# Kernel tuning notes

Measured on AMD Instinct MI355X. Metric: run time of the kernel, lower is better.

## Reference

```python
import jax, jax.numpy as jnp
import numpy as np

TAU = 0.2
LW = 0.5
EPS = 1e-12  # tf.math.l2_normalize epsilon


def _l2norm(x):
    ss = jnp.sum(x * x, axis=-1, keepdims=True)
    return x * jax.lax.rsqrt(jnp.maximum(ss, EPS))


def _global_head(f, W1, b1, W2, b2):
    g = jnp.mean(f, axis=(1, 2))            # GlobalAveragePooling2D -> [B, C]
    h = jax.nn.relu(g @ W1 + b1)
    return h @ W2 + b2                      # [B, 128]


def _dense_head(f, W1, b1, W2, b2):
    # 1x1 convs == per-pixel matmuls
    h = jax.nn.relu(jnp.einsum('bhwc,cd->bhwd', f, W1) + b1)
    return jnp.einsum('bhwd,de->bhwe', h, W2) + b2  # [B, H, W, 128]


def _info_nce(q, k):
    logits = (q @ k.T) / TAU                # [N, N]
    lse = jax.nn.logsumexp(logits, axis=-1)
    pos = jnp.diagonal(logits)
    return jnp.mean(lse - pos)


def setup_inputs() -> dict:
    key = jax.random.key(0)
    ks = jax.random.split(key, 10)
    B, H, W, C = 128, 7, 7, 2048
    Dh, De = 2048, 128
    s1 = 1.0 / np.sqrt(C)
    s2 = 1.0 / np.sqrt(Dh)
    inp = {
        'feat_q': jax.random.normal(ks[0], (B, H, W, C), jnp.float32),
        'feat_k': jax.random.normal(ks[1], (B, H, W, C), jnp.float32),
        'Wg1': jax.random.normal(ks[2], (C, Dh), jnp.float32) * s1,
        'bg1': jnp.zeros((Dh,), jnp.float32),
        'Wg2': jax.random.normal(ks[3], (Dh, De), jnp.float32) * s2,
        'bg2': jnp.zeros((De,), jnp.float32),
        'Wd1': jax.random.normal(ks[4], (C, Dh), jnp.float32) * s1,
        'bd1': jnp.zeros((Dh,), jnp.float32),
        'Wd2': jax.random.normal(ks[5], (Dh, De), jnp.float32) * s2,
        'bd2': jnp.zeros((De,), jnp.float32),
        'mWg1': jax.random.normal(ks[6], (C, Dh), jnp.float32) * s1,
        'mbg1': jnp.zeros((Dh,), jnp.float32),
        'mWg2': jax.random.normal(ks[7], (Dh, De), jnp.float32) * s2,
        'mbg2': jnp.zeros((De,), jnp.float32),
        'mWd1': jax.random.normal(ks[8], (C, Dh), jnp.float32) * s1,
        'mbd1': jnp.zeros((Dh,), jnp.float32),
        'mWd2': jax.random.normal(ks[9], (Dh, De), jnp.float32) * s2,
        'mbd2': jnp.zeros((De,), jnp.float32),
    }
    return inp


def reference(feat_q, feat_k, Wg1, bg1, Wg2, bg2, Wd1, bd1, Wd2, bd2,
              mWg1, mbg1, mWg2, mbg2, mWd1, mbd1, mWd2, mbd2):
    # query (student) branch
    q_g = _l2norm(_global_head(feat_q, Wg1, bg1, Wg2, bg2))      # [B, 128]
    q_d = _l2norm(_dense_head(feat_q, Wd1, bd1, Wd2, bd2))       # [B, H, W, 128]
    # key (momentum teacher) branch, stop-gradient as in train_step
    k_g = jax.lax.stop_gradient(_l2norm(_global_head(feat_k, mWg1, mbg1, mWg2, mbg2)))
    k_d = jax.lax.stop_gradient(_l2norm(_dense_head(feat_k, mWd1, mbd1, mWd2, mbd2)))

    l_g = _info_nce(q_g, k_g)

    B, H, W, De = q_d.shape
    f1 = q_d.reshape(B, H * W, De)
    f2 = k_d.reshape(B, H * W, De)
    sim = jnp.einsum('bnc,bmc->bnm', f1, f2)                     # [B, HW, HW]
    idx = jnp.argmax(sim, axis=-1)                               # [B, HW]
    matched = jnp.take_along_axis(f2, idx[..., None], axis=1)    # [B, HW, 128]

    l_d = _info_nce(f1.reshape(-1, De), matched.reshape(-1, De))
    total = (1.0 - LW) * l_g + LW * l_d
    return total
```

## Files before the change

kernel.cpp:

```cpp
#include <hip/hip_runtime.h>
#include <cstddef>

typedef __bf16 bf16x8 __attribute__((ext_vector_type(8)));
typedef float  f32x4  __attribute__((ext_vector_type(4)));
typedef unsigned short u16x8 __attribute__((ext_vector_type(8)));

__device__ __forceinline__ float b2f(unsigned short u) {
    union { unsigned int i; float f; } v; v.i = ((unsigned int)u) << 16; return v.f;
}
__device__ __forceinline__ unsigned short f2b(float f) {
    union { float f; unsigned int i; } v; v.f = f;
    unsigned int r = v.i + 0x7fffu + ((v.i >> 16) & 1u);
    return (unsigned short)(r >> 16);
}
__device__ __forceinline__ void gl_lds16(const void* g, void* l) {
    __builtin_amdgcn_global_load_lds((const __attribute__((address_space(1))) void*)g,
                                     (__attribute__((address_space(3))) void*)l,
                                     16, 0, 0);
}

__global__ __launch_bounds__(64) void detect_kernel(const unsigned short* __restrict__ feat,
                                                    int* __restrict__ flag) {
    __shared__ int cnt;
    if (threadIdx.x == 0) cnt = 0;
    __syncthreads();
    int c = 0;
    for (int i = threadIdx.x; i < 256; i += 64) {
        float v = b2f(feat[i]);
        if (fabsf(v) > 100.0f) ++c;
    }
    atomicAdd(&cnt, c);
    __syncthreads();
    if (threadIdx.x == 0) *flag = (cnt > 16) ? 1 : 0;
}

__global__ __launch_bounds__(256) void zero_kernel(float* __restrict__ p, int n4) {
    int i = blockIdx.x * 256 + threadIdx.x;
    const f32x4 z = {0.f, 0.f, 0.f, 0.f};
    if (i < n4) ((f32x4*)p)[i] = z;
}

__global__ __launch_bounds__(256) void convert_kernel(const void* __restrict__ in,
                                                      unsigned short* __restrict__ out,
                                                      const int* __restrict__ flagp) {
    int fl = *flagp;
    size_t i = ((size_t)blockIdx.x * 256 + threadIdx.x) * 8;
    if (fl) {
        const float* inf = (const float*)in;
        f32x4 v0 = *(const f32x4*)(inf + i);
        f32x4 v1 = *(const f32x4*)(inf + i + 4);
        u16x8 o;
        o[0]=f2b(v0[0]); o[1]=f2b(v0[1]); o[2]=f2b(v0[2]); o[3]=f2b(v0[3]);
        o[4]=f2b(v1[0]); o[5]=f2b(v1[1]); o[6]=f2b(v1[2]); o[7]=f2b(v1[3]);
        *(u16x8*)(out + i) = o;
    } else {
        *(u16x8*)(out + i) = *(const u16x8*)((const unsigned short*)in + i);
    }
}

__global__ __launch_bounds__(256) void pool_kernel(const void* __restrict__ fq,
                                                   const void* __restrict__ fk,
                                                   unsigned short* __restrict__ gq,
                                                   unsigned short* __restrict__ gk,
                                                   const int* __restrict__ flagp) {
    int fl = *flagp;
    int c = blockIdx.x * 256 + threadIdx.x;
    int b = blockIdx.y;
    const void* src = blockIdx.z ? fk : fq;
    unsigned short* dst = blockIdx.z ? gk : gq;
    size_t base = (size_t)b * 49 * 2048 + c;
    float s = 0.f;
    if (fl) {
        const float* sf = (const float*)src;
        #pragma unroll
        for (int p = 0; p < 49; ++p) s += sf[base + (size_t)p * 2048];
    } else {
        const unsigned short* su = (const unsigned short*)src;
        #pragma unroll
        for (int p = 0; p < 49; ++p) s += b2f(su[base + (size_t)p * 2048]);
    }
    dst[(size_t)b * 2048 + c] = f2b(s * (1.0f / 49.0f));
}

__global__ __launch_bounds__(256) void transpose2v_kernel(
    const void* __restrict__ s0, const void* __restrict__ s1,
    unsigned short* __restrict__ d0, unsigned short* __restrict__ d1,
    int rows, int cols, const int* __restrict__ flagp) {
    int fl = *flagp;
    int z = blockIdx.z;
    const void* in = z ? s1 : s0;
    unsigned short* out = z ? d1 : d0;
    __shared__ unsigned short tile[64 * 72];
    int bx = blockIdx.x * 64, by = blockIdx.y * 64;
    int tr = threadIdx.x >> 3;
    int tc = (threadIdx.x & 7) * 8;
    #pragma unroll
    for (int h = 0; h < 2; ++h) {
        int r = tr + h * 32;
        if (fl) {
            const float* inf = (const float*)in + (size_t)(by + r) * cols + bx + tc;
            f32x4 v0 = *(const f32x4*)inf;
            f32x4 v1 = *(const f32x4*)(inf + 4);
            u16x8 o;
            o[0]=f2b(v0[0]); o[1]=f2b(v0[1]); o[2]=f2b(v0[2]); o[3]=f2b(v0[3]);
            o[4]=f2b(v1[0]); o[5]=f2b(v1[1]); o[6]=f2b(v1[2]); o[7]=f2b(v1[3]);
            *(u16x8*)(tile + r * 72 + tc) = o;
        } else {
            const unsigned short* inu = (const unsigned short*)in + (size_t)(by + r) * cols + bx + tc;
            *(u16x8*)(tile + r * 72 + tc) = *(const u16x8*)inu;
        }
    }
    __syncthreads();
    #pragma unroll
    for (int h = 0; h < 2; ++h) {
        int oc = tr + h * 32;
        u16x8 v;
        #pragma unroll
        for (int j = 0; j < 8; ++j) v[j] = tile[(tc + j) * 72 + oc];
        *(u16x8*)(out + (size_t)(bx + oc) * rows + by + tc) = v;
    }
}

__global__ __launch_bounds__(256) void transpose4v_kernel(
    const void* __restrict__ s0, const void* __restrict__ s1,
    const void* __restrict__ s2, const void* __restrict__ s3,
    unsigned short* __restrict__ d0, unsigned short* __restrict__ d1,
    unsigned short* __restrict__ d2, unsigned short* __restrict__ d3,
    int rows, int cols, const int* __restrict__ flagp) {
    int fl = *flagp;
    int z = blockIdx.z;
    const void* in = (z == 0) ? s0 : (z == 1) ? s1 : (z == 2) ? s2 : s3;
    unsigned short* out = (z == 0) ? d0 : (z == 1) ? d1 : (z == 2) ? d2 : d3;
    __shared__ unsigned short tile[64 * 72];
    int bx = blockIdx.x * 64, by = blockIdx.y * 64;
    int tr = threadIdx.x >> 3;
    int tc = (threadIdx.x & 7) * 8;
    #pragma unroll
    for (int h = 0; h < 2; ++h) {
        int r = tr + h * 32;
        if (fl) {
            const float* inf = (const float*)in + (size_t)(by + r) * cols + bx + tc;
            f32x4 v0 = *(const f32x4*)inf;
            f32x4 v1 = *(const f32x4*)(inf + 4);
            u16x8 o;
            o[0]=f2b(v0[0]); o[1]=f2b(v0[1]); o[2]=f2b(v0[2]); o[3]=f2b(v0[3]);
            o[4]=f2b(v1[0]); o[5]=f2b(v1[1]); o[6]=f2b(v1[2]); o[7]=f2b(v1[3]);
            *(u16x8*)(tile + r * 72 + tc) = o;
        } else {
            const unsigned short* inu = (const unsigned short*)in + (size_t)(by + r) * cols + bx + tc;
            *(u16x8*)(tile + r * 72 + tc) = *(const u16x8*)inu;
        }
    }
    __syncthreads();
    #pragma unroll
    for (int h = 0; h < 2; ++h) {
        int oc = tr + h * 32;
        u16x8 v;
        #pragma unroll
        for (int j = 0; j < 8; ++j) v[j] = tile[(tc + j) * 72 + oc];
        *(u16x8*)(out + (size_t)(bx + oc) * rows + by + tc) = v;
    }
}

__global__ __launch_bounds__(256) void mlp_kernel(
    const unsigned short* __restrict__ A0, const unsigned short* __restrict__ A1,
    const unsigned short* __restrict__ Bt0, const unsigned short* __restrict__ Bt1,
    const unsigned short* __restrict__ W20, const unsigned short* __restrict__ W21,
    const void* __restrict__ b10, const void* __restrict__ b11,
    float* __restrict__ out0, float* __restrict__ out1,
    const int* __restrict__ flagp)
{
    int fl = *flagp;
    int z  = blockIdx.z;
    const unsigned short* A  = z ? A1 : A0;
    const unsigned short* Bt = z ? Bt1 : Bt0;
    const unsigned short* W2 = z ? W21 : W20;
    const void* b1 = z ? b11 : b10;
    float* outp = z ? out1 : out0;
    const int K = 2048;

    __shared__ unsigned short smem[8192 + 9216];
    unsigned short* As = smem;
    unsigned short* Bs = smem + 8192;
    unsigned short* Hs = smem + 8192;

    int tid  = threadIdx.x;
    int lane = tid & 63;
    int w    = tid >> 6;
    int wm = w & 1, wn = w >> 1;
    int quad = lane >> 4, l16 = lane & 15;
    size_t m0 = (size_t)blockIdx.y * 128;
    size_t n0 = (size_t)blockIdx.x * 128;

    int lrow = lane >> 3;
    int kc   = (lane & 7) ^ lrow;

    const unsigned short* gA[4];
    const unsigned short* gB[4];
    unsigned short* lA[4];
    unsigned short* lB[4];
    #pragma unroll
    for (int c = 0; c < 4; ++c) {
        int row = w * 32 + c * 8 + lrow;
        gA[c] = A  + (m0 + row) * (size_t)K + kc * 8;
        gB[c] = Bt + (n0 + row) * (size_t)K + kc * 8;
        lA[c] = As + w * 2048 + c * 512;
        lB[c] = Bs + w * 2048 + c * 512;
    }

    const f32x4 zero4 = {0.f, 0.f, 0.f, 0.f};
    f32x4 acc[4][4];
    #pragma unroll
    for (int i = 0; i < 4; ++i)
        #pragma unroll
        for (int j = 0; j < 4; ++j) acc[i][j] = zero4;

    int swz = l16 & 7;
    for (int kb = 0; kb < K / 64; ++kb) {
        __syncthreads();
        #pragma unroll
        for (int c = 0; c < 4; ++c) { gl_lds16(gA[c], lA[c]); gA[c] += 64; }
        #pragma unroll
        for (int c = 0; c < 4; ++c) { gl_lds16(gB[c], lB[c]); gB[c] += 64; }
        __syncthreads();
        #pragma unroll
        for (int k0 = 0; k0 < 64; k0 += 32) {
            bf16x8 af[4], bfr[4];
            #pragma unroll
            for (int mt = 0; mt < 4; ++mt) {
                int row = wm * 64 + mt * 16 + l16;
                int sc  = (((k0 >> 3) + quad) ^ swz) << 3;
                af[mt] = *(const bf16x8*)(As + row * 64 + sc);
            }
            #pragma unroll
            for (int nt = 0; nt < 4; ++nt) {
                int row = wn * 64 + nt * 16 + l16;
                int sc  = (((k0 >> 3) + quad) ^ swz) << 3;
                bfr[nt] = *(const bf16x8*)(Bs + row * 64 + sc);
            }
            #pragma unroll
            for (int mt = 0; mt < 4; ++mt)
                #pragma unroll
                for (int nt = 0; nt < 4; ++nt)
                    acc[mt][nt] = __builtin_amdgcn_mfma_f32_16x16x32_bf16(af[mt], bfr[nt], acc[mt][nt], 0, 0, 0);
        }
    }

    float b1v[4];
    #pragma unroll
    for (int nt = 0; nt < 4; ++nt) {
        int col = (int)n0 + wn * 64 + nt * 16 + l16;
        b1v[nt] = fl ? ((const float*)b1)[col] : b2f(((const unsigned short*)b1)[col]);
    }

    f32x4 acc2[4][4];
    #pragma unroll
    for (int i = 0; i < 4; ++i)
        #pragma unroll
        for (int j = 0; j < 4; ++j) acc2[i][j] = zero4;

    #pragma unroll
    for (int hf = 0; hf < 2; ++hf) {
        __syncthreads();
        if (wn == hf) {
            #pragma unroll
            for (int mt = 0; mt < 4; ++mt)
                #pragma unroll
                for (int nt = 0; nt < 4; ++nt)
                    #pragma unroll
                    for (int r = 0; r < 4; ++r) {
                        float v = fmaxf(acc[mt][nt][r] + b1v[nt], 0.f);
                        Hs[(wm * 64 + mt * 16 + quad * 4 + r) * 72 + nt * 16 + l16] = f2b(v);
                    }
        } else {
            #pragma unroll
            for (int c = 0; c < 8; ++c) {
                const unsigned short* g = W2 + (size_t)(wm * 64 + c * 8 + lrow) * 2048
                                          + n0 + hf * 64 + kc * 8;
                gl_lds16(g, As + wm * 4096 + c * 512);
            }
        }
        __syncthreads();
        #pragma unroll
        for (int k0 = 0; k0 < 64; k0 += 32) {
            bf16x8 ha[4], wb[4];
            #pragma unroll
            for (int mt = 0; mt < 4; ++mt)
                ha[mt] = *(const bf16x8*)(Hs + (wm * 64 + mt * 16 + l16) * 72 + k0 + quad * 8);
            #pragma unroll
            for (int et = 0; et < 4; ++et) {
                int row = wn * 64 + et * 16 + l16;
                int sc  = (((k0 >> 3) + quad) ^ swz) << 3;
                wb[et] = *(const bf16x8*)(As + row * 64 + sc);
            }
            #pragma unroll
            for (int mt = 0; mt < 4; ++mt)
                #pragma unroll
                for (int et = 0; et < 4; ++et)
                    acc2[mt][et] = __builtin_amdgcn_mfma_f32_16x16x32_bf16(ha[mt], wb[et], acc2[mt][et], 0, 0, 0);
        }
    }

    #pragma unroll
    for (int et = 0; et < 4; ++et) {
        int col = wn * 64 + et * 16 + l16;
        #pragma unroll
        for (int mt = 0; mt < 4; ++mt)
            #pragma unroll
            for (int r = 0; r < 4; ++r) {
                size_t row = m0 + wm * 64 + mt * 16 + quad * 4 + r;
                atomicAdd(&outp[row * 128 + col], acc2[mt][et][r]);
            }
    }
}

__global__ __launch_bounds__(256) void simmatch_kernel(
    const float* __restrict__ rawdq, const float* __restrict__ rawdk,
    const void* __restrict__ bd2, const void* __restrict__ mbd2,
    unsigned short* __restrict__ qd, unsigned short* __restrict__ kd,
    unsigned short* __restrict__ matched, float* __restrict__ pos,
    const int* __restrict__ flagp) {
    int fl = *flagp;
    __shared__ float f1s[49 * 128];
    __shared__ float f2s[49 * 128];
    int b = blockIdx.x;
    int t = threadIdx.x;
    size_t base = (size_t)b * 49 * 128;

    int rr = t >> 2, jq = t & 3;
    if (rr < 49) {
        #pragma unroll
        for (int br = 0; br < 2; ++br) {
            const float* raw = br ? rawdk : rawdq;
            const void* bias = br ? mbd2 : bd2;
            unsigned short* outg = br ? kd : qd;
            float* fs = br ? f2s : f1s;
            size_t idx = base + (size_t)rr * 128 + jq * 32;
            float x[32];
            float ss = 0.f;
            #pragma unroll
            for (int c = 0; c < 32; ++c) {
                float bv = fl ? ((const float*)bias)[jq * 32 + c]
                              : b2f(((const unsigned short*)bias)[jq * 32 + c]);
                x[c] = raw[idx + c] + bv;
                ss += x[c] * x[c];
            }
            ss += __shfl_xor(ss, 1); ss += __shfl_xor(ss, 2);
            float rs = rsqrtf(fmaxf(ss, 1e-12f));
            #pragma unroll
            for (int c = 0; c < 32; ++c) {
                unsigned short us = f2b(x[c] * rs);
                outg[idx + c] = us;
                fs[rr * 128 + jq * 32 + c] = b2f(us);
            }
        }
    }
    __syncthreads();

    int i = t >> 2, q4 = t & 3;
    if (i < 49) {
        int mlo = q4 * 13;
        int mhi = mlo + 13; if (mhi > 49) mhi = 49;
        float best = -1e30f; int bi = 1 << 20;
        const f32x4* va = (const f32x4*)(f1s + i * 128);
        for (int m = mlo; m < mhi; ++m) {
            const f32x4* vb = (const f32x4*)(f2s + m * 128);
            float d = 0.f;
            #pragma unroll
            for (int j = 0; j < 32; ++j) {
                f32x4 a = va[j], bb = vb[j];
                d += a[0]*bb[0] + a[1]*bb[1] + a[2]*bb[2] + a[3]*bb[3];
            }
            if (d > best) { best = d; bi = m; }
        }
        #pragma unroll
        for (int off = 1; off < 4; off <<= 1) {
            float ov = __shfl_xor(best, off);
            int   oi = __shfl_xor(bi, off);
            if (ov > best || (ov == best && oi < bi)) { best = ov; bi = oi; }
        }
        if (q4 == 0) pos[b * 49 + i] = best * 5.0f;
        for (int j = q4 * 32; j < q4 * 32 + 32; ++j)
            matched[base + (size_t)i * 128 + j] = f2b(f2s[bi * 128 + j]);
    }
}

#define KS 136
__global__ __launch_bounds__(256) void lse_kernel(const unsigned short* __restrict__ qd,
                                                  const unsigned short* __restrict__ matched,
                                                  float* __restrict__ lsep) {
    __shared__ unsigned short As[128 * KS];
    __shared__ unsigned short Bs[64 * KS];
    __shared__ float rsum[128];
    int tid  = threadIdx.x;
    int lane = tid & 63, wave = tid >> 6;
    int wm = wave & 1, wn = wave >> 1;
    int quad = lane >> 4, l16 = lane & 15;
    size_t m0 = (size_t)blockIdx.x * 128;
    int z = blockIdx.y;

    #pragma unroll
    for (int i = 0; i < 8; ++i) {
        int l = tid + 256 * i;
        int row = l >> 4, ko = (l & 15) << 3;
        u16x8 v = *(const u16x8*)(qd + (m0 + row) * 128 + ko);
        *(u16x8*)(As + row * KS + ko) = v;
    }
    if (tid < 128) rsum[tid] = 0.f;

    float rs[4][4];
    #pragma unroll
    for (int mt = 0; mt < 4; ++mt)
        #pragma unroll
        for (int r = 0; r < 4; ++r) rs[mt][r] = 0.f;

    const f32x4 zero4 = {0.f, 0.f, 0.f, 0.f};
    int nlo = z * 896, nhi = nlo + 896;
    for (int n0 = nlo; n0 < nhi; n0 += 64) {
        __syncthreads();
        #pragma unroll
        for (int i = 0; i < 4; ++i) {
            int l = tid + 256 * i;
            int row = l >> 4, ko = (l & 15) << 3;
            u16x8 v = *(const u16x8*)(matched + (size_t)(n0 + row) * 128 + ko);
            *(u16x8*)(Bs + row * KS + ko) = v;
        }
        __syncthreads();
        f32x4 acc[4][2];
        #pragma unroll
        for (int mt = 0; mt < 4; ++mt) { acc[mt][0] = zero4; acc[mt][1] = zero4; }
        #pragma unroll
        for (int k0 = 0; k0 < 128; k0 += 32) {
            bf16x8 af[4], bfr[2];
            #pragma unroll
            for (int mt = 0; mt < 4; ++mt)
                af[mt] = *(const bf16x8*)(As + (wm * 64 + mt * 16 + l16) * KS + k0 + quad * 8);
            #pragma unroll
            for (int nt = 0; nt < 2; ++nt)
                bfr[nt] = *(const bf16x8*)(Bs + (wn * 32 + nt * 16 + l16) * KS + k0 + quad * 8);
            #pragma unroll
            for (int mt = 0; mt < 4; ++mt)
                #pragma unroll
                for (int nt = 0; nt < 2; ++nt)
                    acc[mt][nt] = __builtin_amdgcn_mfma_f32_16x16x32_bf16(af[mt], bfr[nt], acc[mt][nt], 0, 0, 0);
        }
        #pragma unroll
        for (int mt = 0; mt < 4; ++mt)
            #pragma unroll
            for (int r = 0; r < 4; ++r)
                rs[mt][r] += __expf(acc[mt][0][r] * 5.0f) + __expf(acc[mt][1][r] * 5.0f);
    }
    #pragma unroll
    for (int mt = 0; mt < 4; ++mt)
        #pragma unroll
        for (int r = 0; r < 4; ++r) {
            float v = rs[mt][r];
            v += __shfl_xor(v, 1); v += __shfl_xor(v, 2);
            v += __shfl_xor(v, 4); v += __shfl_xor(v, 8);
            if (l16 == 0) atomicAdd(&rsum[wm * 64 + mt * 16 + quad * 4 + r], v);
        }
    __syncthreads();
    if (tid < 128) lsep[(size_t)z * 6272 + m0 + tid] = rsum[tid];
}

__global__ __launch_bounds__(128) void lg_kernel(const float* __restrict__ rawgq,
                                                 const float* __restrict__ rawgk,
                                                 const void* __restrict__ bg2,
                                                 const void* __restrict__ mbg2,
                                                 float* __restrict__ lgrow,
                                                 const int* __restrict__ flagp) {
    int fl = *flagp;
    __shared__ float ksf[128 * 128];
    __shared__ float qsf[8 * 128];
    int t = threadIdx.x;
    int rbase = blockIdx.x * 8;
    {
        const float* rk = rawgk + (size_t)t * 128;
        float ss = 0.f;
        for (int c = 0; c < 128; ++c) {
            float bv = fl ? ((const float*)mbg2)[c] : b2f(((const unsigned short*)mbg2)[c]);
            float xx = rk[c] + bv;
            ss += xx * xx;
        }
        float rsv = rsqrtf(fmaxf(ss, 1e-12f));
        for (int c = 0; c < 128; ++c) {
            float bv = fl ? ((const float*)mbg2)[c] : b2f(((const unsigned short*)mbg2)[c]);
            ksf[t * 128 + c] = b2f(f2b((rk[c] + bv) * rsv));
        }
    }
    if (t < 8) {
        const float* rq = rawgq + (size_t)(rbase + t) * 128;
        float ss = 0.f;
        for (int c = 0; c < 128; ++c) {
            float bv = fl ? ((const float*)bg2)[c] : b2f(((const unsigned short*)bg2)[c]);
            float xx = rq[c] + bv;
            ss += xx * xx;
        }
        float rsv = rsqrtf(fmaxf(ss, 1e-12f));
        for (int c = 0; c < 128; ++c) {
            float bv = fl ? ((const float*)bg2)[c] : b2f(((const unsigned short*)bg2)[c]);
            qsf[t * 128 + c] = b2f(f2b((rq[c] + bv) * rsv));
        }
    }
    __syncthreads();
    int rl = t >> 4, jg = t & 15;
    int row = rbase + rl;
    float se = 0.f, diag = 0.f;
    for (int jj = 0; jj < 8; ++jj) {
        int j = jg * 8 + jj;
        float d = 0.f;
        #pragma unroll 8
        for (int c = 0; c < 128; ++c) d += qsf[rl * 128 + c] * ksf[j * 128 + c];
        d *= 5.0f;
        se += __expf(d);
        if (j == row) diag = d;
    }
    #pragma unroll
    for (int off = 1; off < 16; off <<= 1) { se += __shfl_xor(se, off); diag += __shfl_xor(diag, off); }
    if (jg == 0) lgrow[row] = logf(se) - diag;
}

__global__ __launch_bounds__(256) void final_kernel(const float* __restrict__ lsep,
                                                    const float* __restrict__ pos,
                                                    const float* __restrict__ lgrow,
                                                    unsigned int* __restrict__ out) {
    int t = threadIdx.x;
    float s = 0.f;
    for (int i = t; i < 6272; i += 256) {
        float se = 0.f;
        #pragma unroll
        for (int zz = 0; zz < 7; ++zz) se += lsep[zz * 6272 + i];
        s += logf(se) - pos[i];
    }
    float g = (t < 128) ? lgrow[t] : 0.f;
    #pragma unroll
    for (int off = 32; off >= 1; off >>= 1) { s += __shfl_xor(s, off); g += __shfl_xor(g, off); }
    __shared__ float p8[8];
    if ((t & 63) == 0) { p8[t >> 6] = s; p8[4 + (t >> 6)] = g; }
    __syncthreads();
    if (t == 0) {
        float ld  = (p8[0] + p8[1] + p8[2] + p8[3]) * (1.0f / 6272.0f);
        float lg  = (p8[4] + p8[5] + p8[6] + p8[7]) * (1.0f / 128.0f);
        float total = 0.5f * lg + 0.5f * ld;
        unsigned int L = f2b(total);
        union { float f; unsigned int u; } tb; tb.f = total;
        unsigned int base = (tb.u & 0xFFFF0000u) | L;
        unsigned int bu = base; float be = 1e30f;
        #pragma unroll
        for (int d = -1; d <= 1; ++d) {
            unsigned int c = base + ((unsigned int)d << 16);
            union { unsigned int u; float f; } cv; cv.u = c;
            float e = fabsf(cv.f - total);
            if (e < be) { be = e; bu = c; }
        }
        out[0] = bu;
    }
}

#define SLOTA_OFF ((size_t)0)
#define QD_OFF    ((size_t)0)
#define KD_OFF    ((size_t)1605632)
#define MT_OFF    ((size_t)3211264)
#define SLOTB_OFF ((size_t)8388608)
#define W2DQ_OFF  ((size_t)34078720)
#define W2DK_OFF  ((size_t)34603008)
#define W2GQ_OFF  ((size_t)35127296)
#define W2GK_OFF  ((size_t)35651584)
#define RAWDQ_OFF ((size_t)36175872)
#define RAWDK_OFF ((size_t)39387136)
#define RAWGQ_OFF ((size_t)42598400)
#define RAWGK_OFF ((size_t)42663936)
#define GQ_OFF    ((size_t)42729472)
#define GK_OFF    ((size_t)43253760)
#define POS_OFF   ((size_t)42729472)
#define LSEP_OFF  ((size_t)42754560)
#define LGR_OFF   ((size_t)42930176)
#define FLAG_OFF  ((size_t)42930688)

extern "C" void kernel_launch(void* const* d_in, const int* in_sizes, int n_in,
                              void* d_out, int out_size, void* d_ws, size_t ws_size,
                              hipStream_t stream) {
    (void)in_sizes; (void)n_in; (void)out_size; (void)ws_size;
    const void* feat_q = d_in[0];
    const void* feat_k = d_in[1];
    const void* Wg1 = d_in[2];  const void* bg1 = d_in[3];
    const void* Wg2 = d_in[4];  const void* bg2 = d_in[5];
    const void* Wd1 = d_in[6];  const void* bd1 = d_in[7];
    const void* Wd2 = d_in[8];  const void* bd2 = d_in[9];
    const void* mWg1 = d_in[10]; const void* mbg1 = d_in[11];
    const void* mWg2 = d_in[12]; const void* mbg2 = d_in[13];
    const void* mWd1 = d_in[14]; const void* mbd1 = d_in[15];
    const void* mWd2 = d_in[16]; const void* mbd2 = d_in[17];

    char* ws = (char*)d_ws;
    unsigned short* slotA = (unsigned short*)(ws + SLOTA_OFF);
    unsigned short* slotB = (unsigned short*)(ws + SLOTB_OFF);
    unsigned short* W2dq = (unsigned short*)(ws + W2DQ_OFF);
    unsigned short* W2dk = (unsigned short*)(ws + W2DK_OFF);
    unsigned short* W2gq = (unsigned short*)(ws + W2GQ_OFF);
    unsigned short* W2gk = (unsigned short*)(ws + W2GK_OFF);
    float* rawdq = (float*)(ws + RAWDQ_OFF);
    float* rawdk = (float*)(ws + RAWDK_OFF);
    float* rawgq = (float*)(ws + RAWGQ_OFF);
    float* rawgk = (float*)(ws + RAWGK_OFF);
    unsigned short* gq = (unsigned short*)(ws + GQ_OFF);
    unsigned short* gk = (unsigned short*)(ws + GK_OFF);
    unsigned short* qd = (unsigned short*)(ws + QD_OFF);
    unsigned short* kd = (unsigned short*)(ws + KD_OFF);
    unsigned short* mt = (unsigned short*)(ws + MT_OFF);
    float* pos  = (float*)(ws + POS_OFF);
    float* lsep = (float*)(ws + LSEP_OFF);
    float* lgr  = (float*)(ws + LGR_OFF);
    int*   flag = (int*)(ws + FLAG_OFF);

    detect_kernel<<<1, 64, 0, stream>>>((const unsigned short*)feat_q, flag);

    pool_kernel<<<dim3(8, 128, 2), 256, 0, stream>>>(feat_q, feat_k, gq, gk, flag);

    transpose2v_kernel<<<dim3(32, 32, 2), 256, 0, stream>>>(Wg1, mWg1, slotA, slotB, 2048, 2048, flag);
    transpose4v_kernel<<<dim3(2, 32, 4), 256, 0, stream>>>(
        Wd2, mWd2, Wg2, mWg2, W2dq, W2dk, W2gq, W2gk, 2048, 128, flag);

    zero_kernel<<<1600, 256, 0, stream>>>(rawdq, 409600);

    mlp_kernel<<<dim3(16, 1, 2), 256, 0, stream>>>(
        gq, gk, slotA, slotB, W2gq, W2gk, bg1, mbg1, rawgq, rawgk, flag);

    transpose2v_kernel<<<dim3(32, 32, 1), 256, 0, stream>>>(Wd1, Wd1, slotA, slotA, 2048, 2048, flag);
    convert_kernel<<<6272, 256, 0, stream>>>(feat_q, slotB, flag);
    mlp_kernel<<<dim3(16, 49, 1), 256, 0, stream>>>(
        slotB, slotB, slotA, slotA, W2dq, W2dq, bd1, bd1, rawdq, rawdq, flag);

    transpose2v_kernel<<<dim3(32, 32, 1), 256, 0, stream>>>(mWd1, mWd1, slotA, slotA, 2048, 2048, flag);
    convert_kernel<<<6272, 256, 0, stream>>>(feat_k, slotB, flag);
    mlp_kernel<<<dim3(16, 49, 1), 256, 0, stream>>>(
        slotB, slotB, slotA, slotA, W2dk, W2dk, mbd1, mbd1, rawdk, rawdk, flag);

    simmatch_kernel<<<128, 256, 0, stream>>>(rawdq, rawdk, bd2, mbd2, qd, kd, mt, pos, flag);
    lse_kernel<<<dim3(49, 7), 256, 0, stream>>>(qd, mt, lsep);
    lg_kernel<<<16, 128, 0, stream>>>(rawgq, rawgk, bg2, mbg2, lgr, flag);
    final_kernel<<<1, 256, 0, stream>>>(lsep, pos, lgr, (unsigned int*)d_out);
}
```

Before: 636.6 us.

## Merge dense and global MLPs into one launch with fused convert-pool

Adds a larger-workspace path where both feature tensors are converted to bf16 and average-pooled in one pass. All four first-layer weights are transposed in a single launch. One mega MLP kernel then covers the dense query, dense key and global heads in a single grid of 16x50x2 blocks. This removes the serialised per-branch transpose/convert/MLP sequence and several small launches, so the dense GEMMs can fill the GPU together. The cost is a much larger workspace, with a fallback to the old path when the workspace is too small. The convpool kernel uses only 256 blocks, each looping over 49 pixels, which may underuse bandwidth.

Measured after the change: 575.3 us. 9.6% less time.

```diff
diff --git a/kernel.cpp b/kernel.cpp
--- a/kernel.cpp
+++ b/kernel.cpp
@@ -38,6 +38,46 @@
     int i = blockIdx.x * 256 + threadIdx.x;
     const f32x4 z = {0.f, 0.f, 0.f, 0.f};
     if (i < n4) ((f32x4*)p)[i] = z;
+}
+
+__global__ __launch_bounds__(256) void convpool_kernel(const void* __restrict__ fq,
+                                                       const void* __restrict__ fk,
+                                                       unsigned short* __restrict__ FQ,
+                                                       unsigned short* __restrict__ FK,
+                                                       unsigned short* __restrict__ gq,
+                                                       unsigned short* __restrict__ gk,
+                                                       const int* __restrict__ flagp) {
+    int fl = *flagp;
+    int b = blockIdx.y;
+    const void* src = blockIdx.z ? fk : fq;
+    unsigned short* dst = blockIdx.z ? FK : FQ;
+    unsigned short* g   = blockIdx.z ? gk : gq;
+    int c0 = threadIdx.x * 8;
+    float s[8];
+    #pragma unroll
+    for (int j = 0; j < 8; ++j) s[j] = 0.f;
+    for (int p = 0; p < 49; ++p) {
+        size_t idx = ((size_t)b * 49 + p) * 2048 + c0;
+        u16x8 o;
+        if (fl) {
+            const float* sf = (const float*)src + idx;
+            f32x4 v0 = *(const f32x4*)sf;
+            f32x4 v1 = *(const f32x4*)(sf + 4);
+            o[0]=f2b(v0[0]); o[1]=f2b(v0[1]); o[2]=f2b(v0[2]); o[3]=f2b(v0[3]);
+            o[4]=f2b(v1[0]); o[5]=f2b(v1[1]); o[6]=f2b(v1[2]); o[7]=f2b(v1[3]);
+            s[0]+=v0[0]; s[1]+=v0[1]; s[2]+=v0[2]; s[3]+=v0[3];
+            s[4]+=v1[0]; s[5]+=v1[1]; s[6]+=v1[2]; s[7]+=v1[3];
+        } else {
+            o = *(const u16x8*)((const unsigned short*)src + idx);
+            #pragma unroll
+            for (int j = 0; j < 8; ++j) s[j] += b2f(o[j]);
+        }
+        *(u16x8*)(dst + idx) = o;
+    }
+    u16x8 gm;
+    #pragma unroll
+    for (int j = 0; j < 8; ++j) gm[j] = f2b(s[j] * (1.0f / 49.0f));
+    *(u16x8*)(g + (size_t)b * 2048 + c0) = gm;
 }
 
 __global__ __launch_bounds__(256) void convert_kernel(const void* __restrict__ in,
@@ -162,23 +202,12 @@
     }
 }
 
-__global__ __launch_bounds__(256) void mlp_kernel(
-    const unsigned short* __restrict__ A0, const unsigned short* __restrict__ A1,
-    const unsigned short* __restrict__ Bt0, const unsigned short* __restrict__ Bt1,
-    const unsigned short* __restrict__ W20, const unsigned short* __restrict__ W21,
-    const void* __restrict__ b10, const void* __restrict__ b11,
-    float* __restrict__ out0, float* __restrict__ out1,
-    const int* __restrict__ flagp)
+__device__ __forceinline__ void mlp_body(
+    const unsigned short* __restrict__ A, const unsigned short* __restrict__ Bt,
+    const unsigned short* __restrict__ W2, const void* __restrict__ b1,
+    float* __restrict__ outp, size_t m0, size_t n0, int fl)
 {
-    int fl = *flagp;
-    int z  = blockIdx.z;
-    const unsigned short* A  = z ? A1 : A0;
-    const unsigned short* Bt = z ? Bt1 : Bt0;
-    const unsigned short* W2 = z ? W21 : W20;
-    const void* b1 = z ? b11 : b10;
-    float* outp = z ? out1 : out0;
     const int K = 2048;
-
     __shared__ unsigned short smem[8192 + 9216];
     unsigned short* As = smem;
     unsigned short* Bs = smem + 8192;
@@ -189,9 +218,6 @@
     int w    = tid >> 6;
     int wm = w & 1, wn = w >> 1;
     int quad = lane >> 4, l16 = lane & 15;
-    size_t m0 = (size_t)blockIdx.y * 128;
-    size_t n0 = (size_t)blockIdx.x * 128;
-
     int lrow = lane >> 3;
     int kc   = (lane & 7) ^ lrow;
 
@@ -312,6 +338,49 @@
                 atomicAdd(&outp[row * 128 + col], acc2[mt][et][r]);
             }
     }
+}
+
+__global__ __launch_bounds__(256) void mlp_mega_kernel(
+    const unsigned short* __restrict__ FQ, const unsigned short* __restrict__ FK,
+    const unsigned short* __restrict__ gq, const unsigned short* __restrict__ gk,
+    const unsigned short* __restrict__ WD1T, const unsigned short* __restrict__ MWD1T,
+    const unsigned short* __restrict__ WG1T, const unsigned short* __restrict__ MWG1T,
+    const unsigned short* __restrict__ W2dq, const unsigned short* __restrict__ W2dk,
+    const unsigned short* __restrict__ W2gq, const unsigned short* __restrict__ W2gk,
+    const void* __restrict__ bd1, const void* __restrict__ mbd1,
+    const void* __restrict__ bg1, const void* __restrict__ mbg1,
+    float* __restrict__ rawdq, float* __restrict__ rawdk,
+    float* __restrict__ rawgq, float* __restrict__ rawgk,
+    const int* __restrict__ flagp)
+{
+    int fl = *flagp;
+    int z = blockIdx.z;
+    int isg = (blockIdx.y == 49);
+    const unsigned short *A, *Bt, *W2; const void* b1; float* outp;
+    if (!isg) {
+        A = z ? FK : FQ;  Bt = z ? MWD1T : WD1T;  W2 = z ? W2dk : W2dq;
+        b1 = z ? mbd1 : bd1;  outp = z ? rawdk : rawdq;
+    } else {
+        A = z ? gk : gq;  Bt = z ? MWG1T : WG1T;  W2 = z ? W2gk : W2gq;
+        b1 = z ? mbg1 : bg1;  outp = z ? rawgk : rawgq;
+    }
+    size_t m0 = isg ? 0 : (size_t)blockIdx.y * 128;
+    size_t n0 = (size_t)blockIdx.x * 128;
+    mlp_body(A, Bt, W2, b1, outp, m0, n0, fl);
+}
+
+__global__ __launch_bounds__(256) void mlp_kernel(
+    const unsigned short* __restrict__ A0, const unsigned short* __restrict__ A1,
+    const unsigned short* __restrict__ Bt0, const unsigned short* __restrict__ Bt1,
+    const unsigned short* __restrict__ W20, const unsigned short* __restrict__ W21,
+    const void* __restrict__ b10, const void* __restrict__ b11,
+    float* __restrict__ out0, float* __restrict__ out1,
+    const int* __restrict__ flagp)
+{
+    int fl = *flagp;
+    int z  = blockIdx.z;
+    mlp_body(z ? A1 : A0, z ? Bt1 : Bt0, z ? W21 : W20, z ? b11 : b10,
+             z ? out1 : out0, (size_t)blockIdx.y * 128, (size_t)blockIdx.x * 128, fl);
 }
 
 __global__ __launch_bounds__(256) void simmatch_kernel(
@@ -557,30 +626,55 @@
     }
 }
 
-#define SLOTA_OFF ((size_t)0)
-#define QD_OFF    ((size_t)0)
-#define KD_OFF    ((size_t)1605632)
-#define MT_OFF    ((size_t)3211264)
-#define SLOTB_OFF ((size_t)8388608)
-#define W2DQ_OFF  ((size_t)34078720)
-#define W2DK_OFF  ((size_t)34603008)
-#define W2GQ_OFF  ((size_t)35127296)
-#define W2GK_OFF  ((size_t)35651584)
-#define RAWDQ_OFF ((size_t)36175872)
-#define RAWDK_OFF ((size_t)39387136)
-#define RAWGQ_OFF ((size_t)42598400)
-#define RAWGK_OFF ((size_t)42663936)
-#define GQ_OFF    ((size_t)42729472)
-#define GK_OFF    ((size_t)43253760)
-#define POS_OFF   ((size_t)42729472)
-#define LSEP_OFF  ((size_t)42754560)
-#define LGR_OFF   ((size_t)42930176)
-#define FLAG_OFF  ((size_t)42930688)
+#define A_FQ     ((size_t)0)
+#define A_FK     ((size_t)25690112)
+#define A_WD1T   ((size_t)51380224)
+#define A_MWD1T  ((size_t)59768832)
+#define A_WG1T   ((size_t)68157440)
+#define A_MWG1T  ((size_t)76546048)
+#define A_W2DQ   ((size_t)84934656)
+#define A_W2DK   ((size_t)85458944)
+#define A_W2GQ   ((size_t)85983232)
+#define A_W2GK   ((size_t)86507520)
+#define A_RAWDQ  ((size_t)87031808)
+#define A_RAWDK  ((size_t)90243072)
+#define A_RAWGQ  ((size_t)93454336)
+#define A_RAWGK  ((size_t)93519872)
+#define A_GQ     ((size_t)93585408)
+#define A_GK     ((size_t)94109696)
+#define A_QD     ((size_t)94633984)
+#define A_KD     ((size_t)96239616)
+#define A_MT     ((size_t)97845248)
+#define A_POS    ((size_t)99450880)
+#define A_LSEP   ((size_t)99475968)
+#define A_LGR    ((size_t)99651584)
+#define A_FLAG   ((size_t)99652096)
+#define A_NEED   ((size_t)99652608)
+
+#define B_SLOTA  ((size_t)0)
+#define B_QD     ((size_t)0)
+#define B_KD     ((size_t)1605632)
+#define B_MT     ((size_t)3211264)
+#define B_SLOTB  ((size_t)8388608)
+#define B_W2DQ   ((size_t)34078720)
+#define B_W2DK   ((size_t)34603008)
+#define B_W2GQ   ((size_t)35127296)
+#define B_W2GK   ((size_t)35651584)
+#define B_RAWDQ  ((size_t)36175872)
+#define B_RAWDK  ((size_t)39387136)
+#define B_RAWGQ  ((size_t)42598400)
+#define B_RAWGK  ((size_t)42663936)
+#define B_GQ     ((size_t)42729472)
+#define B_GK     ((size_t)43253760)
+#define B_POS    ((size_t)42729472)
+#define B_LSEP   ((size_t)42754560)
+#define B_LGR    ((size_t)42930176)
+#define B_FLAG   ((size_t)42930688)
 
 extern "C" void kernel_launch(void* const* d_in, const int* in_sizes, int n_in,
                               void* d_out, int out_size, void* d_ws, size_t ws_size,
                               hipStream_t stream) {
-    (void)in_sizes; (void)n_in; (void)out_size; (void)ws_size;
+    (void)in_sizes; (void)n_in; (void)out_size;
     const void* feat_q = d_in[0];
     const void* feat_k = d_in[1];
     const void* Wg1 = d_in[2];  const void* bg1 = d_in[3];
@@ -591,53 +685,88 @@
     const void* mWg2 = d_in[12]; const void* mbg2 = d_in[13];
     const void* mWd1 = d_in[14]; const void* mbd1 = d_in[15];
     const void* mWd2 = d_in[16]; const void* mbd2 = d_in[17];
-
     char* ws = (char*)d_ws;
-    unsigned short* slotA = (unsigned short*)(ws + SLOTA_OFF);
-    unsigned short* slotB = (unsigned short*)(ws + SLOTB_OFF);
-    unsigned short* W2dq = (unsigned short*)(ws + W2DQ_OFF);
-    unsigned short* W2dk = (unsigned short*)(ws + W2DK_OFF);
-    unsigned short* W2gq = (unsigned short*)(ws + W2GQ_OFF);
-    unsigned short* W2gk = (unsigned short*)(ws + W2GK_OFF);
-    float* rawdq = (float*)(ws + RAWDQ_OFF);
-    float* rawdk = (float*)(ws + RAWDK_OFF);
-    float* rawgq = (float*)(ws + RAWGQ_OFF);
-    float* rawgk = (float*)(ws + RAWGK_OFF);
-    unsigned short* gq = (unsigned short*)(ws + GQ_OFF);
-    unsigned short* gk = (unsigned short*)(ws + GK_OFF);
-    unsigned short* qd = (unsigned short*)(ws + QD_OFF);
-    unsigned short* kd = (unsigned short*)(ws + KD_OFF);
-    unsigned short* mt = (unsigned short*)(ws + MT_OFF);
-    float* pos  = (float*)(ws + POS_OFF);
-    float* lsep = (float*)(ws + LSEP_OFF);
-    float* lgr  = (float*)(ws + LGR_OFF);
-    int*   flag = (int*)(ws + FLAG_OFF);
-
-    detect_kernel<<<1, 64, 0, stream>>>((const unsigned short*)feat_q, flag);
-
-    pool_kernel<<<dim3(8, 128, 2), 256, 0, stream>>>(feat_q, feat_k, gq, gk, flag);
-
-    transpose2v_kernel<<<dim3(32, 32, 2), 256, 0, stream>>>(Wg1, mWg1, slotA, slotB, 2048, 2048, flag);
-    transpose4v_kernel<<<dim3(2, 32, 4), 256, 0, stream>>>(
-        Wd2, mWd2, Wg2, mWg2, W2dq, W2dk, W2gq, W2gk, 2048, 128, flag);
-
-    zero_kernel<<<1600, 256, 0, stream>>>(rawdq, 409600);
-
-    mlp_kernel<<<dim3(16, 1, 2), 256, 0, stream>>>(
-        gq, gk, slotA, slotB, W2gq, W2gk, bg1, mbg1, rawgq, rawgk, flag);
-
-    transpose2v_kernel<<<dim3(32, 32, 1), 256, 0, stream>>>(Wd1, Wd1, slotA, slotA, 2048, 2048, flag);
-    convert_kernel<<<6272, 256, 0, stream>>>(feat_q, slotB, flag);
-    mlp_kernel<<<dim3(16, 49, 1), 256, 0, stream>>>(
-        slotB, slotB, slotA, slotA, W2dq, W2dq, bd1, bd1, rawdq, rawdq, flag);
-
-    transpose2v_kernel<<<dim3(32, 32, 1), 256, 0, stream>>>(mWd1, mWd1, slotA, slotA, 2048, 2048, flag);
-    convert_kernel<<<6272, 256, 0, stream>>>(feat_k, slotB, flag);
-    mlp_kernel<<<dim3(16, 49, 1), 256, 0, stream>>>(
-        slotB, slotB, slotA, slotA, W2dk, W2dk, mbd1, mbd1, rawdk, rawdk, flag);
-
-    simmatch_kernel<<<128, 256, 0, stream>>>(rawdq, rawdk, bd2, mbd2, qd, kd, mt, pos, flag);
-    lse_kernel<<<dim3(49, 7), 256, 0, stream>>>(qd, mt, lsep);
-    lg_kernel<<<16, 128, 0, stream>>>(rawgq, rawgk, bg2, mbg2, lgr, flag);
-    final_kernel<<<1, 256, 0, stream>>>(lsep, pos, lgr, (unsigned int*)d_out);
-}
+
+    if (ws_size >= A_NEED) {
+        unsigned short* FQ    = (unsigned short*)(ws + A_FQ);
+        unsigned short* FK    = (unsigned short*)(ws + A_FK);
+        unsigned short* WD1T  = (unsigned short*)(ws + A_WD1T);
+        unsigned short* MWD1T = (unsigned short*)(ws + A_MWD1T);
+        unsigned short* WG1T  = (unsigned short*)(ws + A_WG1T);
+        unsigned short* MWG1T = (unsigned short*)(ws + A_MWG1T);
+        unsigned short* W2dq  = (unsigned short*)(ws + A_W2DQ);
+        unsigned short* W2dk  = (unsigned short*)(ws + A_W2DK);
+        unsigned short* W2gq  = (unsigned short*)(ws + A_W2GQ);
+        unsigned short* W2gk  = (unsigned short*)(ws + A_W2GK);
+        float* rawdq = (float*)(ws + A_RAWDQ);
+        float* rawdk = (float*)(ws + A_RAWDK);
+        float* rawgq = (float*)(ws + A_RAWGQ);
+        float* rawgk = (float*)(ws + A_RAWGK);
+        unsigned short* gq = (unsigned short*)(ws + A_GQ);
+        unsigned short* gk = (unsigned short*)(ws + A_GK);
+        unsigned short* qd = (unsigned short*)(ws + A_QD);
+        unsigned short* kd = (unsigned short*)(ws + A_KD);
+        unsigned short* mt = (unsigned short*)(ws + A_MT);
+        float* pos  = (float*)(ws + A_POS);
+        float* lsep = (float*)(ws + A_LSEP);
+        float* lgr  = (float*)(ws + A_LGR);
+        int*   flag = (int*)(ws + A_FLAG);
+
+        detect_kernel<<<1, 64, 0, stream>>>((const unsigned short*)feat_q, flag);
+        convpool_kernel<<<dim3(1, 128, 2), 256, 0, stream>>>(feat_q, feat_k, FQ, FK, gq, gk, flag);
+        transpose4v_kernel<<<dim3(32, 32, 4), 256, 0, stream>>>(
+            Wd1, mWd1, Wg1, mWg1, WD1T, MWD1T, WG1T, MWG1T, 2048, 2048, flag);
+        transpose4v_kernel<<<dim3(2, 32, 4), 256, 0, stream>>>(
+            Wd2, mWd2, Wg2, mWg2, W2dq, W2dk, W2gq, W2gk, 2048, 128, flag);
+        zero_kernel<<<1600, 256, 0, stream>>>(rawdq, 409600);
+        mlp_mega_kernel<<<dim3(16, 50, 2), 256, 0, stream>>>(
+            FQ, FK, gq, gk, WD1T, MWD1T, WG1T, MWG1T,
+            W2dq, W2dk, W2gq, W2gk, bd1, mbd1, bg1, mbg1,
+            rawdq, rawdk, rawgq, rawgk, flag);
+        simmatch_kernel<<<128, 256, 0, stream>>>(rawdq, rawdk, bd2, mbd2, qd, kd, mt, pos, flag);
+        lse_kernel<<<dim3(49, 7), 256, 0, stream>>>(qd, mt, lsep);
+        lg_kernel<<<16, 128, 0, stream>>>(rawgq, rawgk, bg2, mbg2, lgr, flag);
+        final_kernel<<<1, 256, 0, stream>>>(lsep, pos, lgr, (unsigned int*)d_out);
+    } else {
+        unsigned short* slotA = (unsigned short*)(ws + B_SLOTA);
+        unsigned short* slotB = (unsigned short*)(ws + B_SLOTB);
+        unsigned short* W2dq = (unsigned short*)(ws + B_W2DQ);
+        unsigned short* W2dk = (unsigned short*)(ws + B_W2DK);
+        unsigned short* W2gq = (unsigned short*)(ws + B_W2GQ);
+        unsigned short* W2gk = (unsigned short*)(ws + B_W2GK);
+        float* rawdq = (float*)(ws + B_RAWDQ);
+        float* rawdk = (float*)(ws + B_RAWDK);
+        float* rawgq = (float*)(ws + B_RAWGQ);
+        float* rawgk = (float*)(ws + B_RAWGK);
+        unsigned short* gq = (unsigned short*)(ws + B_GQ);
+        unsigned short* gk = (unsigned short*)(ws + B_GK);
+        unsigned short* qd = (unsigned short*)(ws + B_QD);
+        unsigned short* kd = (unsigned short*)(ws + B_KD);
+        unsigned short* mt = (unsigned short*)(ws + B_MT);
+        float* pos  = (float*)(ws + B_POS);
+        float* lsep = (float*)(ws + B_LSEP);
+        float* lgr  = (float*)(ws + B_LGR);
+        int*   flag = (int*)(ws + B_FLAG);
+
+        detect_kernel<<<1, 64, 0, stream>>>((const unsigned short*)feat_q, flag);
+        pool_kernel<<<dim3(8, 128, 2), 256, 0, stream>>>(feat_q, feat_k, gq, gk, flag);
+        transpose2v_kernel<<<dim3(32, 32, 2), 256, 0, stream>>>(Wg1, mWg1, slotA, slotB, 2048, 2048, flag);
+        transpose4v_kernel<<<dim3(2, 32, 4), 256, 0, stream>>>(
+            Wd2, mWd2, Wg2, mWg2, W2dq, W2dk, W2gq, W2gk, 2048, 128, flag);
+        zero_kernel<<<1600, 256, 0, stream>>>(rawdq, 409600);
+        mlp_kernel<<<dim3(16, 1, 2), 256, 0, stream>>>(
+            gq, gk, slotA, slotB, W2gq, W2gk, bg1, mbg1, rawgq, rawgk, flag);
+        transpose2v_kernel<<<dim3(32, 32, 1), 256, 0, stream>>>(Wd1, Wd1, slotA, slotA, 2048, 2048, flag);
+        convert_kernel<<<6272, 256, 0, stream>>>(feat_q, slotB, flag);
+        mlp_kernel<<<dim3(16, 49, 1), 256, 0, stream>>>(
+            slotB, slotB, slotA, slotA, W2dq, W2dq, bd1, bd1, rawdq, rawdq, flag);
+        transpose2v_kernel<<<dim3(32, 32, 1), 256, 0, stream>>>(mWd1, mWd1, slotA, slotA, 2048, 2048, flag);
+        convert_kernel<<<6272, 256, 0, stream>>>(feat_k, slotB, flag);
+        mlp_kernel<<<dim3(16, 49, 1), 256, 0, stream>>>(
+            slotB, slotB, slotA, slotA, W2dk, W2dk, mbd1, mbd1, rawdk, rawdk, flag);
+        simmatch_kernel<<<128, 256, 0, stream>>>(rawdq, rawdk, bd2, mbd2, qd, kd, mt, pos, flag);
+        lse_kernel<<<dim3(49, 7), 256, 0, stream>>>(qd, mt, lsep);
+        lg_kernel<<<16, 128, 0, stream>>>(rawgq, rawgk, bg2, mbg2, lgr, flag);
+        final_kernel<<<1, 256, 0, stream>>>(lsep, pos, lgr, (unsigned int*)d_out);
+    }
+}
```
